# Performance work log

Hardware: AMD Instinct MI355X
Metric: run time of the kernel (lower is better)

The kernel has to match this reference:

```python
import jax, jax.numpy as jnp
import numpy as np

N_EMBD = 1024
N_HEAD = 16
HEAD_DIM = N_EMBD // N_HEAD  # 64
R = 8
D_STD = HEAD_DIM - R         # 56
BLOCK_SIZE = 2048
B, T = 2, 2048
NEG = -1e9


def setup_inputs() -> dict:
    key = jax.random.key(0)
    ks = jax.random.split(key, 8)
    x = jax.random.normal(ks[0], (B, T, N_EMBD), dtype=jnp.float32)
    Wqkv = jax.random.normal(ks[1], (3 * N_EMBD, N_EMBD), dtype=jnp.float32) * 0.02
    Wproj = jax.random.normal(ks[2], (N_EMBD, N_EMBD), dtype=jnp.float32) * 0.02
    W_recip = jax.random.normal(ks[3], (HEAD_DIM, R), dtype=jnp.float32) * 0.02
    # mixing weights must be positive (sqrt is taken); match init scale
    w_std = jnp.full((N_HEAD,), 0.5, dtype=jnp.float32)
    w_rec = jnp.full((N_HEAD,), 0.3, dtype=jnp.float32)  # > threshold -> all heads RA
    w_disc = jnp.full((N_HEAD,), 0.2, dtype=jnp.float32)
    d_bias = jax.random.normal(ks[4], (N_HEAD, BLOCK_SIZE), dtype=jnp.float32) * 0.02
    return {"x": x, "Wqkv": Wqkv, "Wproj": Wproj, "W_recip": W_recip,
            "w_std": w_std, "w_rec": w_rec, "w_disc": w_disc, "d_bias": d_bias}


def reference(x, Wqkv, Wproj, W_recip, w_std, w_rec, w_disc, d_bias):
    Bx, Tx, C = x.shape
    H, hd = N_HEAD, HEAD_DIM
    qkv = x @ Wqkv.T                                   # (B,T,3C)
    q, k, v = jnp.split(qkv, 3, axis=-1)
    def heads(t):
        return t.reshape(Bx, Tx, H, hd).transpose(0, 2, 1, 3)  # (B,H,T,hd)
    q, k, v = heads(q), heads(k), heads(v)
    q_low = jnp.einsum('bhtd,dr->bhtr', q, W_recip)    # (B,H,T,R)
    k_low = jnp.einsum('bhtd,dr->bhtr', k, W_recip)
    sw_std = jnp.sqrt(w_std)[None, :, None, None]
    sw_rec = jnp.sqrt(w_rec)[None, :, None, None]
    # cross augmentation: q side carries k_low, k side carries q_low
    q_aug = jnp.concatenate([sw_std * q[..., :D_STD], sw_rec * k_low], axis=-1)
    k_aug = jnp.concatenate([sw_std * k[..., :D_STD], sw_rec * q_low], axis=-1)
    scale = 1.0 / jnp.sqrt(jnp.asarray(hd, dtype=x.dtype))
    scores = jnp.einsum('bhqd,bhkd->bhqk', q_aug, k_aug) * scale
    # per-head learned bias over key positions, broadcast over queries
    bias = w_disc[None, :, None, None] * d_bias[:, :Tx][None, :, None, :]
    scores = scores + bias
    causal = jnp.tril(jnp.ones((Tx, Tx), dtype=bool))
    scores = jnp.where(causal[None, None], scores, NEG)
    attn = jax.nn.softmax(scores, axis=-1)
    out = jnp.einsum('bhqk,bhkd->bhqd', attn, v)       # (B,H,T,hd)
    out = out.transpose(0, 2, 1, 3).reshape(Bx, Tx, C)
    return out @ Wproj.T
```

## Files before the change

kernel.cpp:

```cpp
#include <hip/hip_runtime.h>
#include <math.h>

#define T_SEQ 2048
#define NH 16
#define HD 64
#define CEMB 1024
#define NEGINF -3.0e38f
#define LOG2E 1.4426950408889634f

typedef unsigned short ushort;
typedef unsigned int uint;
typedef __attribute__((ext_vector_type(8))) short short8;
typedef __attribute__((ext_vector_type(4))) float f32x4;

#if __has_builtin(__builtin_amdgcn_exp2f)
#define EXP2(x) __builtin_amdgcn_exp2f(x)
#else
#define EXP2(x) exp2f(x)
#endif

__device__ __forceinline__ float b2f(ushort h) {
    union { uint u; float f; } cv; cv.u = ((uint)h) << 16; return cv.f;
}
__device__ __forceinline__ ushort f2b(float f) {
    union { float f; uint u; } cv; cv.f = f;
    return (ushort)((cv.u + 0x7FFF + ((cv.u >> 16) & 1)) >> 16);
}
__device__ __forceinline__ ushort f2b_fast(float f) {
    union { float f; uint u; } cv; cv.f = f;
    return (ushort)((cv.u + 0x8000) >> 16);
}
__device__ __forceinline__ uint pack_bf16(float a, float b) {
    union { float f; uint u; } ua, ub; ua.f = a; ub.f = b;
    return __builtin_amdgcn_perm(ub.u + 0x8000u, ua.u + 0x8000u, 0x07060302u);
}
__device__ __forceinline__ void gl2lds16(const ushort* g, ushort* l) {
    __builtin_amdgcn_global_load_lds(
        (const __attribute__((address_space(1))) void*)g,
        (__attribute__((address_space(3))) void*)l, 16, 0, 0);
}

__global__ __launch_bounds__(256) void prep_kernel(
    const float* __restrict__ x, const float* __restrict__ Wqkv,
    const float* __restrict__ Wproj, const float* __restrict__ W_recip,
    const float* __restrict__ w_disc, const float* __restrict__ d_bias,
    ushort* __restrict__ xb, ushort* __restrict__ wqkvb,
    ushort* __restrict__ wprojb, float* __restrict__ bias_pre)
{
    const int bid = blockIdx.x;
    if (bid >= 48) {
        const int off0 = bid - 48;
        const float* src; ushort* dst; int off;
        if (off0 < 4096)      { src = x;     dst = xb;     off = off0; }
        else if (off0 < 7168) { src = Wqkv;  dst = wqkvb;  off = off0 - 4096; }
        else                  { src = Wproj; dst = wprojb; off = off0 - 7168; }
        const int i = (off * 256 + threadIdx.x) * 4;
        const float4 v = *(const float4*)&src[i];
        ushort4 o;
        o.x = f2b(v.x); o.y = f2b(v.y); o.z = f2b(v.z); o.w = f2b(v.w);
        *(ushort4*)&dst[i] = o;
        return;
    }
    if (bid >= 32) {
        const int h = bid - 32;
        const float wd = w_disc[h] * LOG2E;
        const int j = h * T_SEQ + threadIdx.x * 8;
        const float4 a = *(const float4*)&d_bias[j];
        const float4 c = *(const float4*)&d_bias[j + 4];
        float4 oa, oc;
        oa.x = a.x * wd; oa.y = a.y * wd; oa.z = a.z * wd; oa.w = a.w * wd;
        oc.x = c.x * wd; oc.y = c.y * wd; oc.z = c.z * wd; oc.w = c.w * wd;
        *(float4*)&bias_pre[j] = oa;
        *(float4*)&bias_pre[j + 4] = oc;
        return;
    }
    const int qk = bid >> 4, h = bid & 15;
    const int e0 = threadIdx.x * 4;
    f32x4 acc[8];
    #pragma unroll
    for (int r = 0; r < 8; ++r) acc[r] = (f32x4){0.f, 0.f, 0.f, 0.f};
    #pragma unroll 4
    for (int d = 0; d < 64; ++d) {
        const float4 xv = *(const float4*)&Wqkv[(size_t)(qk * 1024 + h * 64 + d) * 1024 + e0];
        #pragma unroll
        for (int r = 0; r < 8; ++r) {
            const float w = W_recip[d * 8 + r];
            acc[r][0] = fmaf(w, xv.x, acc[r][0]);
            acc[r][1] = fmaf(w, xv.y, acc[r][1]);
            acc[r][2] = fmaf(w, xv.z, acc[r][2]);
            acc[r][3] = fmaf(w, xv.w, acc[r][3]);
        }
    }
    #pragma unroll
    for (int r = 0; r < 8; ++r) {
        ushort4 o;
        o.x = f2b(acc[r][0]); o.y = f2b(acc[r][1]);
        o.z = f2b(acc[r][2]); o.w = f2b(acc[r][3]);
        *(ushort4*)&wqkvb[(size_t)(3072 + qk * 128 + h * 8 + r) * 1024 + e0] = o;
    }
}

#define GEMM_CORE(Aptr, Bptr, KDIM, SMEMN)                                     \
    __shared__ __align__(16) ushort SMEM[SMEMN];                               \
    ushort* const Asl = SMEM;                                                  \
    ushort* const Bsl = SMEM + 8192;                                           \
    const int row0 = blockIdx.x * 128;                                         \
    const int col0 = blockIdx.y * 128;                                         \
    const int tid = threadIdx.x;                                               \
    const int wave = tid >> 6, lane = tid & 63;                                \
    const int wm = wave >> 1, wn = wave & 1;                                   \
    const int quad = lane >> 4, lq = lane & 15;                                \
    const int l7 = lq & 7;                                                     \
    f32x4 acc[4][4];                                                           \
    _Pragma("unroll") for (int i = 0; i < 4; ++i)                              \
        _Pragma("unroll") for (int j = 0; j < 4; ++j)                          \
            acc[i][j] = (f32x4){0.f, 0.f, 0.f, 0.f};                           \
    for (int k0 = 0; k0 < (KDIM); k0 += 64) {                                  \
        _Pragma("unroll") for (int p = 0; p < 4; ++p) {                        \
            const int idx = p * 256 + tid;                                     \
            const int row = idx >> 3, slot = idx & 7;                          \
            const int kc = (slot ^ (row & 7)) << 3;                            \
            gl2lds16(&(Aptr)[(size_t)(row0 + row) * (KDIM) + k0 + kc], &Asl[idx * 8]); \
            gl2lds16(&(Bptr)[(size_t)(col0 + row) * (KDIM) + k0 + kc], &Bsl[idx * 8]); \
        }                                                                      \
        __syncthreads();                                                       \
        _Pragma("unroll") for (int ks = 0; ks < 2; ++ks) {                     \
            short8 af[4], bf[4];                                               \
            _Pragma("unroll") for (int i = 0; i < 4; ++i)                      \
                af[i] = *(const short8*)&Asl[(wm * 64 + i * 16 + lq) * 64 +    \
                                             (((ks * 4 + quad) ^ l7) << 3)];   \
            _Pragma("unroll") for (int j = 0; j < 4; ++j)                      \
                bf[j] = *(const short8*)&Bsl[(wn * 64 + j * 16 + lq) * 64 +    \
                                             (((ks * 4 + quad) ^ l7) << 3)];   \
            _Pragma("unroll") for (int i = 0; i < 4; ++i)                      \
                _Pragma("unroll") for (int j = 0; j < 4; ++j)                  \
                    acc[i][j] = __builtin_amdgcn_mfma_f32_16x16x32_bf16(       \
                        af[i], bf[j], acc[i][j], 0, 0, 0);                     \
        }                                                                      \
        __syncthreads();                                                       \
    }

#define CSTR 144
__global__ __launch_bounds__(256, 4) void gemm_qkv_kernel(
    const ushort* __restrict__ A, const ushort* __restrict__ Bt,
    const float* __restrict__ w_std, const float* __restrict__ w_rec,
    ushort* __restrict__ qh, ushort* __restrict__ kh, ushort* __restrict__ vt)
{
    GEMM_CORE(A, Bt, 1024, 128 * CSTR)
    ushort* const Cs = SMEM;

    if (col0 >= 2048 && col0 < 3072) {
        #pragma unroll
        for (int j = 0; j < 4; ++j) {
            const int cc = col0 + wn * 64 + j * 16 + lq;
            const int h = (cc >> 6) & 15;
            const int d = cc & 63;
            #pragma unroll
            for (int i = 0; i < 4; ++i) {
                const int rr0 = row0 + wm * 64 + i * 16 + quad * 4;
                const int b = rr0 >> 11, t0 = rr0 & 2047;
                ushort4 pv;
                pv.x = f2b(acc[i][j][0]); pv.y = f2b(acc[i][j][1]);
                pv.z = f2b(acc[i][j][2]); pv.w = f2b(acc[i][j][3]);
                *(ushort4*)&vt[((((size_t)b * NH + h) * HD + d) * T_SEQ + t0)] = pv;
            }
        }
    } else if (col0 < 2048) {
        const bool isq = (col0 < 1024);
        #pragma unroll
        for (int j = 0; j < 4; ++j) {
            const int colc = wn * 64 + j * 16 + lq;
            const int h = ((col0 + colc) >> 6) & 15;
            const float sc = isq ? w_std[h] * (0.125f * LOG2E) : 1.0f;
            #pragma unroll
            for (int i = 0; i < 4; ++i)
                #pragma unroll
                for (int r = 0; r < 4; ++r)
                    Cs[(wm * 64 + i * 16 + quad * 4 + r) * CSTR + colc] =
                        f2b(acc[i][j][r] * sc);
        }
        __syncthreads();
        ushort* dst = isq ? qh : kh;
        const int hbase = (col0 >> 6) & 15;
        #pragma unroll
        for (int rep = 0; rep < 8; ++rep) {
            const int id = rep * 256 + tid;
            const int row = id >> 4, chunk = id & 15;
            if ((chunk & 7) == 7) continue;
            const int h = hbase + (chunk >> 3);
            const int d = (chunk & 7) * 8;
            const int rr = row0 + row;
            const int b = rr >> 11, t = rr & 2047;
            const uint4 val = *(const uint4*)&Cs[row * CSTR + chunk * 8];
            *(uint4*)&dst[((((size_t)b * NH + h) * T_SEQ + t) * HD + d)] = val;
        }
    } else {
        const bool isqlow = (col0 < 3200);
        #pragma unroll
        for (int j = 0; j < 4; ++j) {
            const int colc = wn * 64 + j * 16 + lq;
            const int h = colc >> 3;
            const float sc = isqlow ? 1.0f : w_rec[h] * (0.125f * LOG2E);
            #pragma unroll
            for (int i = 0; i < 4; ++i)
                #pragma unroll
                for (int r = 0; r < 4; ++r)
                    Cs[(wm * 64 + i * 16 + quad * 4 + r) * CSTR + colc] =
                        f2b(acc[i][j][r] * sc);
        }
        __syncthreads();
        ushort* dst = isqlow ? kh : qh;
        #pragma unroll
        for (int rep = 0; rep < 8; ++rep) {
            const int id = rep * 256 + tid;
            const int row = id >> 4, h = id & 15;
            const int rr = row0 + row;
            const int b = rr >> 11, t = rr & 2047;
            const uint4 val = *(const uint4*)&Cs[row * CSTR + h * 8];
            *(uint4*)&dst[((((size_t)b * NH + h) * T_SEQ + t) * HD + 56)] = val;
        }
    }
}

__global__ __launch_bounds__(256, 4) void gemm_proj_kernel(
    const ushort* __restrict__ A, const ushort* __restrict__ Bt,
    float* __restrict__ C)
{
    __shared__ __align__(16) ushort SMEM[12288];
    ushort* const Asl = SMEM;
    ushort* const Bsl = SMEM + 8192;
    const int row0 = blockIdx.x * 128;
    const int col0 = blockIdx.y * 64;
    const int tid = threadIdx.x;
    const int wave = tid >> 6, lane = tid & 63;
    const int quad = lane >> 4, lq = lane & 15;
    const int l7 = lq & 7;
    f32x4 acc[2][4];
    #pragma unroll
    for (int i = 0; i < 2; ++i)
        #pragma unroll
        for (int j = 0; j < 4; ++j)
            acc[i][j] = (f32x4){0.f, 0.f, 0.f, 0.f};

    for (int k0 = 0; k0 < 1024; k0 += 64) {
        #pragma unroll
        for (int p = 0; p < 4; ++p) {
            const int idx = p * 256 + tid;
            const int row = idx >> 3, slot = idx & 7;
            const int kc = (slot ^ (row & 7)) << 3;
            gl2lds16(&A[(size_t)(row0 + row) * 1024 + k0 + kc], &Asl[idx * 8]);
        }
        #pragma unroll
        for (int p = 0; p < 2; ++p) {
            const int idx = p * 256 + tid;
            const int row = idx >> 3, slot = idx & 7;
            const int kc = (slot ^ (row & 7)) << 3;
            gl2lds16(&Bt[(size_t)(col0 + row) * 1024 + k0 + kc], &Bsl[idx * 8]);
        }
        __syncthreads();
        #pragma unroll
        for (int ks = 0; ks < 2; ++ks) {
            short8 af[2], bf[4];
            #pragma unroll
            for (int i = 0; i < 2; ++i)
                af[i] = *(const short8*)&Asl[(wave * 32 + i * 16 + lq) * 64 +
                                             (((ks * 4 + quad) ^ l7) << 3)];
            #pragma unroll
            for (int j = 0; j < 4; ++j)
                bf[j] = *(const short8*)&Bsl[(j * 16 + lq) * 64 +
                                             (((ks * 4 + quad) ^ l7) << 3)];
            #pragma unroll
            for (int i = 0; i < 2; ++i)
                #pragma unroll
                for (int j = 0; j < 4; ++j)
                    acc[i][j] = __builtin_amdgcn_mfma_f32_16x16x32_bf16(
                        af[i], bf[j], acc[i][j], 0, 0, 0);
        }
        __syncthreads();
    }
    #pragma unroll
    for (int i = 0; i < 2; ++i) {
        #pragma unroll
        for (int r = 0; r < 4; ++r) {
            const int rr = row0 + wave * 32 + i * 16 + quad * 4 + r;
            #pragma unroll
            for (int j = 0; j < 4; ++j) {
                const int cc = col0 + j * 16 + lq;
                C[(size_t)rr * 1024 + cc] = acc[i][j][r];
            }
        }
    }
}

#define TILE_COMPUTE(bq, o4, lsum, qrow, NTL) do {                            \
    f32x4 s4[8];                                                              \
    _Pragma("unroll") for (int nt = 0; nt < (NTL); ++nt)                      \
        s4[nt] = *(const f32x4*)&bias_h[k0 + nt * 16 + quad * 4];             \
    __builtin_amdgcn_s_setprio(1);                                            \
    _Pragma("unroll") for (int ks = 0; ks < 2; ++ks)                          \
        _Pragma("unroll") for (int nt = 0; nt < (NTL); ++nt) {                \
            const short8 ak = *(const short8*)                                \
                &Ks[(nt * 16 + lq) * 64 + (((ks * 4 + quad) ^ l7) << 3)];     \
            s4[nt] = __builtin_amdgcn_mfma_f32_16x16x32_bf16(                 \
                ak, (bq)[ks], s4[nt], 0, 0, 0);                               \
        }                                                                     \
    __builtin_amdgcn_s_setprio(0);                                            \
    _Pragma("unroll") for (int nt = 0; nt < (NTL); ++nt) {                    \
        f32x4 sv = s4[nt];                                                    \
        const int kb = k0 + nt * 16 + quad * 4;                               \
        _Pragma("unroll") for (int r = 0; r < 4; ++r)                         \
            if (kb + r > (qrow)) sv[r] = NEGINF;                              \
        const float p0 = EXP2(sv[0]), p1 = EXP2(sv[1]);                       \
        const float p2 = EXP2(sv[2]), p3 = EXP2(sv[3]);                       \
        (lsum) += (p0 + p1) + (p2 + p3);                                      \
        const int pcol = (nt * 16 + quad * 4) ^ (l7 << 3);                    \
        uint2 pv; pv.x = pack_bf16(p0, p1); pv.y = pack_bf16(p2, p3);         \
        *(uint2*)&Ps[prow + pcol] = pv;                                       \
    }                                                                         \
    __builtin_amdgcn_s_setprio(1);                                            \
    _Pragma("unroll") for (int ks = 0; ks < (NTL) / 2; ++ks) {                \
        const short8 bp = *(const short8*)                                    \
            &Ps[prow + ((ks * 32 + quad * 8) ^ (l7 << 3))];                   \
        _Pragma("unroll") for (int dt = 0; dt < 4; ++dt) {                    \
            const short8 bv = *(const short8*)                                \
                &Vs[(dt * 16 + lq) * 128 + (((ks * 4 + quad) ^ lq) << 3)];    \
            (o4)[dt] = __builtin_amdgcn_mfma_f32_16x16x32_bf16(               \
                bv, bp, (o4)[dt], 0, 0, 0);                                   \
        }                                                                     \
    }                                                                         \
    __builtin_amdgcn_s_setprio(0);                                            \
} while (0)

__global__ __launch_bounds__(256, 2) void attn_kernel(
    const ushort* __restrict__ qa, const ushort* __restrict__ ka,
    const ushort* __restrict__ vt, const float* __restrict__ bias_pre,
    ushort* __restrict__ out)
{
    __shared__ __align__(16) ushort Qs[2 * 64 * 64];
    __shared__ __align__(16) ushort Ks[128 * 64];
    __shared__ __align__(16) ushort Ps[64 * 128];
    __shared__ __align__(16) ushort Vs[64 * 128];
    const int bh = blockIdx.x;
    const int qtA = blockIdx.y;
    const int qtB = 31 - blockIdx.y;
    const int h = bh & 15, b = bh >> 4;
    const int tid = threadIdx.x;
    const int wave = tid >> 6, lane = tid & 63;
    const int quad = lane >> 4, lq = lane & 15;
    const int l7 = lq & 7;
    const size_t base = (size_t)bh * T_SEQ * HD;

    #pragma unroll
    for (int rep = 0; rep < 2; ++rep) {
        const int idx = rep * 256 + tid;
        const int row = idx >> 3, slot = idx & 7;
        const int kc = (slot ^ (row & 7)) << 3;
        gl2lds16(&qa[base + (size_t)(qtA * 64 + row) * 64 + kc], &Qs[idx * 8]);
        gl2lds16(&qa[base + (size_t)(qtB * 64 + row) * 64 + kc], &Qs[4096 + idx * 8]);
    }
    __syncthreads();
    short8 bqA[2], bqB[2];
    #pragma unroll
    for (int ks = 0; ks < 2; ++ks) {
        const int off = (wave * 16 + lq) * 64 + (((ks * 4 + quad) ^ l7) << 3);
        bqA[ks] = *(const short8*)&Qs[off];
        bqB[ks] = *(const short8*)&Qs[4096 + off];
    }

    f32x4 o4A[4], o4B[4];
    #pragma unroll
    for (int dt = 0; dt < 4; ++dt) {
        o4A[dt] = (f32x4){0.f, 0.f, 0.f, 0.f};
        o4B[dt] = (f32x4){0.f, 0.f, 0.f, 0.f};
    }
    float lsumA = 0.f, lsumB = 0.f;
    const int qrowA = qtA * 64 + wave * 16 + lq;
    const int qrowB = qtB * 64 + wave * 16 + lq;
    const int prow = (wave * 16 + lq) * 128;
    const int nA = (qtA + 2) >> 1, nB = (qtB + 2) >> 1;
    const float* bias_h = &bias_pre[h * T_SEQ];

    for (int c = 0; c < nB; ++c) {
        const int k0 = c * 128;
        if (c) __syncthreads();
        #pragma unroll
        for (int rep = 0; rep < 4; ++rep) {
            const int idx = rep * 256 + tid;
            const int row = idx >> 3, slot = idx & 7;
            gl2lds16(&ka[base + (size_t)(k0 + row) * 64 + ((slot ^ (row & 7)) << 3)],
                     &Ks[idx * 8]);
        }
        #pragma unroll
        for (int rep = 0; rep < 4; ++rep) {
            const int idx = rep * 256 + tid;
            const int row = idx >> 4, slot = idx & 15;
            gl2lds16(&vt[base + (size_t)row * T_SEQ + k0 + ((slot ^ (row & 15)) << 3)],
                     &Vs[idx * 8]);
        }
        __syncthreads();

        if (c == nB - 1 && !(qtB & 1)) TILE_COMPUTE(bqB, o4B, lsumB, qrowB, 4);
        else                           TILE_COMPUTE(bqB, o4B, lsumB, qrowB, 8);
        if (c < nA) {
            if (c == nA - 1 && !(qtA & 1)) TILE_COMPUTE(bqA, o4A, lsumA, qrowA, 4);
            else                           TILE_COMPUTE(bqA, o4A, lsumA, qrowA, 8);
        }
    }

    lsumA += __shfl_xor(lsumA, 16, 64);
    lsumA += __shfl_xor(lsumA, 32, 64);
    lsumB += __shfl_xor(lsumB, 16, 64);
    lsumB += __shfl_xor(lsumB, 32, 64);
    const float invA = 1.0f / lsumA, invB = 1.0f / lsumB;
    const size_t obaseA = ((size_t)b * T_SEQ + qrowA) * CEMB + h * HD;
    const size_t obaseB = ((size_t)b * T_SEQ + qrowB) * CEMB + h * HD;
    #pragma unroll
    for (int dt = 0; dt < 4; ++dt) {
        ushort4 ov;
        ov.x = f2b_fast(o4A[dt][0] * invA);
        ov.y = f2b_fast(o4A[dt][1] * invA);
        ov.z = f2b_fast(o4A[dt][2] * invA);
        ov.w = f2b_fast(o4A[dt][3] * invA);
        *(ushort4*)&out[obaseA + dt * 16 + quad * 4] = ov;
        ushort4 ow;
        ow.x = f2b_fast(o4B[dt][0] * invB);
        ow.y = f2b_fast(o4B[dt][1] * invB);
        ow.z = f2b_fast(o4B[dt][2] * invB);
        ow.w = f2b_fast(o4B[dt][3] * invB);
        *(ushort4*)&out[obaseB + dt * 16 + quad * 4] = ow;
    }
}

extern "C" void kernel_launch(void* const* d_in, const int* in_sizes, int n_in,
                              void* d_out, int out_size, void* d_ws, size_t ws_size,
                              hipStream_t stream) {
    const float* x       = (const float*)d_in[0];
    const float* Wqkv    = (const float*)d_in[1];
    const float* Wproj   = (const float*)d_in[2];
    const float* W_recip = (const float*)d_in[3];
    const float* w_std   = (const float*)d_in[4];
    const float* w_rec   = (const float*)d_in[5];
    const float* w_disc  = (const float*)d_in[6];
    const float* d_bias  = (const float*)d_in[7];
    float* out = (float*)d_out;

    const size_t NX = (size_t)4096 * 1024;
    const size_t NWQKVX = (size_t)3328 * 1024;
    const size_t NWPROJ = (size_t)1024 * 1024;
    ushort* xb     = (ushort*)d_ws;
    ushort* wqkvb  = xb + NX;
    ushort* wprojb = wqkvb + NWQKVX;
    ushort* qh     = wprojb + NWPROJ;
    ushort* kh     = qh + NX;
    ushort* vt     = kh + NX;
    ushort* ao     = vt + NX;
    float*  bias_pre = (float*)(ao + NX);

    prep_kernel<<<8240, 256, 0, stream>>>(x, Wqkv, Wproj, W_recip, w_disc, d_bias,
                                          xb, wqkvb, wprojb, bias_pre);
    gemm_qkv_kernel<<<dim3(32, 26), 256, 0, stream>>>(xb, wqkvb, w_std, w_rec, qh, kh, vt);
    attn_kernel<<<dim3(32, 16), 256, 0, stream>>>(qh, kh, vt, bias_pre, ao);
    gemm_proj_kernel<<<dim3(32, 16), 256, 0, stream>>>(ao, wprojb, out);
}
```

Baseline: 180.9 us.

## Compact QKV weights to skip unused q/k dims, MFMA row sums, mask only diagonal tiles

The bf16 Wqkv copy now keeps only the first 56 dims per head of q and k, plus the full v rows and the fused low-rank rows. This shrinks the QKV GEMM from 26 to 24 column tiles and makes the scatter epilogue map columns to heads by division by 56. In attention, the softmax denominator is accumulated by an extra MFMA against a vector of ones instead of scalar adds followed by shuffles. The causal mask comparison now runs only on the last, diagonal tile. The extra MFMA per step adds matrix work, and the sums now come from bf16-rounded probabilities, which changes numerics slightly.

```diff
diff --git a/kernel.cpp b/kernel.cpp
--- a/kernel.cpp
+++ b/kernel.cpp
@@ -50,15 +50,35 @@
     const int bid = blockIdx.x;
     if (bid >= 48) {
         const int off0 = bid - 48;
-        const float* src; ushort* dst; int off;
-        if (off0 < 4096)      { src = x;     dst = xb;     off = off0; }
-        else if (off0 < 7168) { src = Wqkv;  dst = wqkvb;  off = off0 - 4096; }
-        else                  { src = Wproj; dst = wprojb; off = off0 - 7168; }
-        const int i = (off * 256 + threadIdx.x) * 4;
-        const float4 v = *(const float4*)&src[i];
-        ushort4 o;
-        o.x = f2b(v.x); o.y = f2b(v.y); o.z = f2b(v.z); o.w = f2b(v.w);
-        *(ushort4*)&dst[i] = o;
+        const int e = threadIdx.x * 4;
+        if (off0 < 4096) {
+            const float4 v = *(const float4*)&x[(size_t)off0 * 1024 + e];
+            ushort4 o;
+            o.x = f2b(v.x); o.y = f2b(v.y); o.z = f2b(v.z); o.w = f2b(v.w);
+            *(ushort4*)&xb[(size_t)off0 * 1024 + e] = o;
+        } else if (off0 < 6912) {
+            const int r = off0 - 4096;
+            int src_row;
+            if (r < 1792) {
+                const int qk = (r >= 896) ? 1 : 0;
+                const int rr = r - qk * 896;
+                const int h = rr / 56;
+                const int d = rr - h * 56;
+                src_row = qk * 1024 + h * 64 + d;
+            } else {
+                src_row = 2048 + (r - 1792);
+            }
+            const float4 v = *(const float4*)&Wqkv[(size_t)src_row * 1024 + e];
+            ushort4 o;
+            o.x = f2b(v.x); o.y = f2b(v.y); o.z = f2b(v.z); o.w = f2b(v.w);
+            *(ushort4*)&wqkvb[(size_t)r * 1024 + e] = o;
+        } else {
+            const int r = off0 - 6912;
+            const float4 v = *(const float4*)&Wproj[(size_t)r * 1024 + e];
+            ushort4 o;
+            o.x = f2b(v.x); o.y = f2b(v.y); o.z = f2b(v.z); o.w = f2b(v.w);
+            *(ushort4*)&wprojb[(size_t)r * 1024 + e] = o;
+        }
         return;
     }
     if (bid >= 32) {
@@ -96,7 +116,7 @@
         ushort4 o;
         o.x = f2b(acc[r][0]); o.y = f2b(acc[r][1]);
         o.z = f2b(acc[r][2]); o.w = f2b(acc[r][3]);
-        *(ushort4*)&wqkvb[(size_t)(3072 + qk * 128 + h * 8 + r) * 1024 + e0] = o;
+        *(ushort4*)&wqkvb[(size_t)(2816 + qk * 128 + h * 8 + r) * 1024 + e0] = o;
     }
 }
 
@@ -149,10 +169,10 @@
     GEMM_CORE(A, Bt, 1024, 128 * CSTR)
     ushort* const Cs = SMEM;
 
-    if (col0 >= 2048 && col0 < 3072) {
+    if (col0 >= 1792 && col0 < 2816) {
         #pragma unroll
         for (int j = 0; j < 4; ++j) {
-            const int cc = col0 + wn * 64 + j * 16 + lq;
+            const int cc = (col0 - 1792) + wn * 64 + j * 16 + lq;
             const int h = (cc >> 6) & 15;
             const int d = cc & 63;
             #pragma unroll
@@ -165,12 +185,13 @@
                 *(ushort4*)&vt[((((size_t)b * NH + h) * HD + d) * T_SEQ + t0)] = pv;
             }
         }
-    } else if (col0 < 2048) {
-        const bool isq = (col0 < 1024);
+    } else if (col0 < 1792) {
+        const bool isq = (col0 < 896);
+        const int cbase = col0 - (isq ? 0 : 896);
         #pragma unroll
         for (int j = 0; j < 4; ++j) {
             const int colc = wn * 64 + j * 16 + lq;
-            const int h = ((col0 + colc) >> 6) & 15;
+            const int h = (cbase + colc) / 56;
             const float sc = isq ? w_std[h] * (0.125f * LOG2E) : 1.0f;
             #pragma unroll
             for (int i = 0; i < 4; ++i)
@@ -181,21 +202,20 @@
         }
         __syncthreads();
         ushort* dst = isq ? qh : kh;
-        const int hbase = (col0 >> 6) & 15;
         #pragma unroll
         for (int rep = 0; rep < 8; ++rep) {
             const int id = rep * 256 + tid;
             const int row = id >> 4, chunk = id & 15;
-            if ((chunk & 7) == 7) continue;
-            const int h = hbase + (chunk >> 3);
-            const int d = (chunk & 7) * 8;
+            const int gidx = cbase + chunk * 8;
+            const int h = gidx / 56;
+            const int d = gidx - h * 56;
             const int rr = row0 + row;
             const int b = rr >> 11, t = rr & 2047;
             const uint4 val = *(const uint4*)&Cs[row * CSTR + chunk * 8];
             *(uint4*)&dst[((((size_t)b * NH + h) * T_SEQ + t) * HD + d)] = val;
         }
     } else {
-        const bool isqlow = (col0 < 3200);
+        const bool isqlow = (col0 < 2944);
         #pragma unroll
         for (int j = 0; j < 4; ++j) {
             const int colc = wn * 64 + j * 16 + lq;
@@ -292,7 +312,7 @@
     }
 }
 
-#define TILE_COMPUTE(bq, o4, lsum, qrow, NTL) do {                            \
+#define TILE_COMPUTE(bq, o4, osum, qrow, NTL, MASK) do {                      \
     f32x4 s4[8];                                                              \
     _Pragma("unroll") for (int nt = 0; nt < (NTL); ++nt)                      \
         s4[nt] = *(const f32x4*)&bias_h[k0 + nt * 16 + quad * 4];             \
@@ -307,12 +327,13 @@
     __builtin_amdgcn_s_setprio(0);                                            \
     _Pragma("unroll") for (int nt = 0; nt < (NTL); ++nt) {                    \
         f32x4 sv = s4[nt];                                                    \
-        const int kb = k0 + nt * 16 + quad * 4;                               \
-        _Pragma("unroll") for (int r = 0; r < 4; ++r)                         \
-            if (kb + r > (qrow)) sv[r] = NEGINF;                              \
+        if (MASK) {                                                           \
+            const int kb = k0 + nt * 16 + quad * 4;                           \
+            _Pragma("unroll") for (int r = 0; r < 4; ++r)                     \
+                if (kb + r > (qrow)) sv[r] = NEGINF;                          \
+        }                                                                     \
         const float p0 = EXP2(sv[0]), p1 = EXP2(sv[1]);                       \
         const float p2 = EXP2(sv[2]), p3 = EXP2(sv[3]);                       \
-        (lsum) += (p0 + p1) + (p2 + p3);                                      \
         const int pcol = (nt * 16 + quad * 4) ^ (l7 << 3);                    \
         uint2 pv; pv.x = pack_bf16(p0, p1); pv.y = pack_bf16(p2, p3);         \
         *(uint2*)&Ps[prow + pcol] = pv;                                       \
@@ -327,6 +348,8 @@
             (o4)[dt] = __builtin_amdgcn_mfma_f32_16x16x32_bf16(               \
                 bv, bp, (o4)[dt], 0, 0, 0);                                   \
         }                                                                     \
+        (osum) = __builtin_amdgcn_mfma_f32_16x16x32_bf16(                     \
+            vones, bp, (osum), 0, 0, 0);                                      \
     }                                                                         \
     __builtin_amdgcn_s_setprio(0);                                            \
 } while (0)
@@ -350,6 +373,10 @@
     const int l7 = lq & 7;
     const size_t base = (size_t)bh * T_SEQ * HD;
 
+    short8 vones;
+    #pragma unroll
+    for (int i = 0; i < 8; ++i) vones[i] = (short)0x3F80;
+
     #pragma unroll
     for (int rep = 0; rep < 2; ++rep) {
         const int idx = rep * 256 + tid;
@@ -368,12 +395,13 @@
     }
 
     f32x4 o4A[4], o4B[4];
+    f32x4 osumA = (f32x4){0.f, 0.f, 0.f, 0.f};
+    f32x4 osumB = (f32x4){0.f, 0.f, 0.f, 0.f};
     #pragma unroll
     for (int dt = 0; dt < 4; ++dt) {
         o4A[dt] = (f32x4){0.f, 0.f, 0.f, 0.f};
         o4B[dt] = (f32x4){0.f, 0.f, 0.f, 0.f};
     }
-    float lsumA = 0.f, lsumB = 0.f;
     const int qrowA = qtA * 64 + wave * 16 + lq;
     const int qrowB = qtB * 64 + wave * 16 + lq;
     const int prow = (wave * 16 + lq) * 128;
@@ -399,19 +427,24 @@
         }
         __syncthreads();
 
-        if (c == nB - 1 && !(qtB & 1)) TILE_COMPUTE(bqB, o4B, lsumB, qrowB, 4);
-        else                           TILE_COMPUTE(bqB, o4B, lsumB, qrowB, 8);
+        if (c == nB - 1) {
+            if (!(qtB & 1)) TILE_COMPUTE(bqB, o4B, osumB, qrowB, 4, 1);
+            else            TILE_COMPUTE(bqB, o4B, osumB, qrowB, 8, 1);
+        } else {
+            TILE_COMPUTE(bqB, o4B, osumB, qrowB, 8, 0);
+        }
         if (c < nA) {
-            if (c == nA - 1 && !(qtA & 1)) TILE_COMPUTE(bqA, o4A, lsumA, qrowA, 4);
-            else                           TILE_COMPUTE(bqA, o4A, lsumA, qrowA, 8);
-        }
-    }
-
-    lsumA += __shfl_xor(lsumA, 16, 64);
-    lsumA += __shfl_xor(lsumA, 32, 64);
-    lsumB += __shfl_xor(lsumB, 16, 64);
-    lsumB += __shfl_xor(lsumB, 32, 64);
-    const float invA = 1.0f / lsumA, invB = 1.0f / lsumB;
+            if (c == nA - 1) {
+                if (!(qtA & 1)) TILE_COMPUTE(bqA, o4A, osumA, qrowA, 4, 1);
+                else            TILE_COMPUTE(bqA, o4A, osumA, qrowA, 8, 1);
+            } else {
+                TILE_COMPUTE(bqA, o4A, osumA, qrowA, 8, 0);
+            }
+        }
+    }
+
+    const float invA = 1.0f / osumA[0];
+    const float invB = 1.0f / osumB[0];
     const size_t obaseA = ((size_t)b * T_SEQ + qrowA) * CEMB + h * HD;
     const size_t obaseB = ((size_t)b * T_SEQ + qrowB) * CEMB + h * HD;
     #pragma unroll
@@ -445,7 +478,7 @@
     float* out = (float*)d_out;
 
     const size_t NX = (size_t)4096 * 1024;
-    const size_t NWQKVX = (size_t)3328 * 1024;
+    const size_t NWQKVX = (size_t)3072 * 1024;
     const size_t NWPROJ = (size_t)1024 * 1024;
     ushort* xb     = (ushort*)d_ws;
     ushort* wqkvb  = xb + NX;
@@ -456,9 +489,9 @@
     ushort* ao     = vt + NX;
     float*  bias_pre = (float*)(ao + NX);
 
-    prep_kernel<<<8240, 256, 0, stream>>>(x, Wqkv, Wproj, W_recip, w_disc, d_bias,
+    prep_kernel<<<7984, 256, 0, stream>>>(x, Wqkv, Wproj, W_recip, w_disc, d_bias,
                                           xb, wqkvb, wprojb, bias_pre);
-    gemm_qkv_kernel<<<dim3(32, 26), 256, 0, stream>>>(xb, wqkvb, w_std, w_rec, qh, kh, vt);
+    gemm_qkv_kernel<<<dim3(32, 24), 256, 0, stream>>>(xb, wqkvb, w_std, w_rec, qh, kh, vt);
     attn_kernel<<<dim3(32, 16), 256, 0, stream>>>(qh, kh, vt, bias_pre, ao);
     gemm_proj_kernel<<<dim3(32, 16), 256, 0, stream>>>(ao, wprojb, out);
 }
```

Measured after the change: 175.3 us (median of 2 runs). 1.03x faster.
